# Performance work log

Hardware: AMD Instinct MI355X
Metric: run time of the kernel (lower is better)

Reference implementation:

```python
import jax, jax.numpy as jnp
import numpy as np

B, S, T = 512, 1024, 50


def setup_inputs() -> dict:
    key = jax.random.key(0)
    k1, k2, k3, k4, k5, k6, k7 = jax.random.split(key, 7)
    token_scores = jax.random.normal(k1, (B, S, T), dtype=jnp.float32)
    tags = jax.random.randint(k2, (B, S), 0, T, dtype=jnp.int64)
    # left-contiguous mask: each sequence has a random valid length >= 1
    lengths = jax.random.randint(k3, (B,), 1, S + 1)
    token_mask = (jnp.arange(S)[None, :] < lengths[:, None]).astype(jnp.int32)
    transitions = jax.random.normal(k4, (T, T), dtype=jnp.float32) * 0.1
    start_transitions = jax.random.normal(k5, (T,), dtype=jnp.float32) * 0.1
    end_transitions = jax.random.normal(k6, (T,), dtype=jnp.float32) * 0.1
    return {
        "token_scores": token_scores,
        "tags": tags,
        "token_mask": token_mask,
        "transitions": transitions,
        "start_transitions": start_transitions,
        "end_transitions": end_transitions,
    }


def _crf_log_likelihood(token_scores, tags, token_mask, transitions,
                        start_transitions, end_transitions):
    # token_scores: [B,S,T], tags: [B,S] int, token_mask: [B,S] {0,1}
    maskf = token_mask.astype(token_scores.dtype)
    maskb = token_mask.astype(bool)

    # ---- numerator: score of the gold tag path ----
    emit = jnp.take_along_axis(token_scores, tags[..., None], axis=2)[..., 0]  # [B,S]
    emit_sum = jnp.sum(emit * maskf, axis=1)
    trans_sum = jnp.sum(transitions[tags[:, :-1], tags[:, 1:]] * maskf[:, 1:], axis=1)
    start_score = start_transitions[tags[:, 0]]
    last_idx = jnp.sum(token_mask, axis=1).astype(jnp.int32) - 1          # [B]
    last_tags = jnp.take_along_axis(tags, last_idx[:, None], axis=1)[:, 0]
    end_score = end_transitions[last_tags]
    numerator = start_score + emit_sum + trans_sum + end_score            # [B]

    # ---- denominator: log partition via forward algorithm (scan over time) ----
    alpha0 = start_transitions[None, :] + token_scores[:, 0]              # [B,T]
    logits_rest = jnp.swapaxes(token_scores[:, 1:], 0, 1)                 # [S-1,B,T]
    mask_rest = jnp.swapaxes(maskb[:, 1:], 0, 1)                          # [S-1,B]

    def step(alpha, xs):
        logit_t, m_t = xs                                                 # [B,T], [B]
        # inner[b, i, j] = alpha[b,i] + transitions[i,j] + logit_t[b,j]
        inner = alpha[:, :, None] + transitions[None, :, :] + logit_t[:, None, :]
        new_alpha = jax.nn.logsumexp(inner, axis=1)                       # [B,T]
        alpha = jnp.where(m_t[:, None], new_alpha, alpha)
        return alpha, None

    alpha, _ = jax.lax.scan(step, alpha0, (logits_rest, mask_rest))
    denominator = jax.nn.logsumexp(alpha + end_transitions[None, :], axis=1)  # [B]

    return jnp.sum(numerator - denominator)  # scalar, summed over batch


def reference(token_scores, tags, token_mask, transitions,
              start_transitions, end_transitions):
    batch_size = token_scores.shape[0]
    ll = _crf_log_likelihood(token_scores, tags, token_mask, transitions,
                             start_transitions, end_transitions)
    return -ll / float(batch_size)
```

## Files before the change

kernel.cpp:

```cpp
#include <hip/hip_runtime.h>
#include <math.h>

#define CB 512
#define CS 1024
#define CT 50
#define PF 4

typedef float v2f __attribute__((ext_vector_type(2)));

#if __has_builtin(__builtin_amdgcn_permlane16_swap)
#define HAVE_PL16 1
#else
#define HAVE_PL16 0
#endif
#if __has_builtin(__builtin_amdgcn_permlane32_swap)
#define HAVE_PL32 1
#else
#define HAVE_PL32 0
#endif

__global__ void zero_out_kernel(float* out) { out[0] = 0.0f; }

__device__ __forceinline__ int lane0_bits(float v) {
    return __builtin_amdgcn_readlane(__float_as_int(v), 0);
}

template <int CTRL>
__device__ __forceinline__ float dppmov(float v) {
    return __int_as_float(__builtin_amdgcn_update_dpp(
        0, __float_as_int(v), CTRL, 0xf, 0xf, false));
}

__device__ __forceinline__ void expand32(float &a, float &b, int lane) {
#if HAVE_PL32
    (void)lane;
    auto r = __builtin_amdgcn_permlane32_swap(__float_as_uint(a), __float_as_uint(a),
                                              false, false);
    a = __uint_as_float(r[0]);
    b = __uint_as_float(r[1]);
#else
    b = __int_as_float(__builtin_amdgcn_ds_bpermute((lane ^ 32) << 2,
                                                    __float_as_int(a)));
#endif
}

__device__ __forceinline__ void expand16(float &a, float &b, int lane) {
    (void)lane;
#if HAVE_PL16
    auto r = __builtin_amdgcn_permlane16_swap(__float_as_uint(a), __float_as_uint(a),
                                              false, false);
    a = __uint_as_float(r[0]);
    b = __uint_as_float(r[1]);
#else
    b = __int_as_float(__builtin_amdgcn_ds_swizzle(__float_as_int(a), 0x401F));
#endif
}

__global__ __launch_bounds__(128, 1) void crf_scan_kernel(
    const float* __restrict__ scores,
    const int*   __restrict__ tags,
    const int*   __restrict__ mask,
    const float* __restrict__ trans,
    const float* __restrict__ start_tr,
    const float* __restrict__ end_tr,
    float* __restrict__ out)
{
    const int b    = blockIdx.x;
    const int tid  = threadIdx.x;
    const int w    = tid >> 6;
    const int lane = tid & 63;
    const int xl   = (lane < CT) ? lane : 0;
    const bool sel4 = (lane & 4) != 0;
    const bool sel8 = (lane & 8) != 0;

    __shared__ __attribute__((aligned(16))) float sTrans[CT * CT];
    __shared__ float sA[64];
    __shared__ float sB[64];
    __shared__ float sLZ[2], sN[2];

    for (int k = tid; k < CT * CT; k += 128) sTrans[k] = trans[k];
    __syncthreads();

    const int F16   = HAVE_PL16 ? (lane & 16) : 0;
    const int F32   = HAVE_PL32 ? (lane & 32) : 0;
    const int sbase = 16 * (lane >> 4) + (lane & 3);

    v2f EC0[16], EC1[16];
    #pragma unroll
    for (int k = 0; k < 16; ++k) {
        const int i = lane
            ^ ((k & 1) ? (32 ^ F32) : F32)
            ^ ((k & 2) ? (16 ^ F16) : F16)
            ^ ((k & 4) ? 1 : 0)
            ^ ((k & 8) ? 2 : 0);
        float e[4];
        #pragma unroll
        for (int u = 0; u < 4; ++u) {
            const int s = sbase + 4 * u;
            e[u] = (i < CT && s < CT)
                 ? __expf(w == 0 ? sTrans[i * CT + s] : sTrans[s * CT + i])
                 : 0.f;
        }
        EC0[k] = (v2f){e[0], e[1]};
        EC1[k] = (v2f){e[2], e[3]};
    }

    const int* mrow = mask + (size_t)b * CS;
    int len = 0;
    for (int t = lane; t < CS; t += 64) len += mrow[t];
    #pragma unroll
    for (int off = 32; off; off >>= 1) len += __shfl_xor(len, off);

    const float* srow = scores + (size_t)b * CS * CT;
    const float* sx   = srow + xl;

    const int tm    = (len - 1) >> 1;
    const int count = (w == 0) ? tm : ((len >= 2) ? (len - 2 - tm) : 0);
    const int base  = (w == 0) ? 1 : (len - 2);
    const int dir   = (w == 0) ? 1 : -1;

    float st;
    if (w == 0) {
        st = (lane < CT) ? __expf(start_tr[lane] + sx[0]) : 0.f;
    } else {
        st = (lane < CT)
            ? ((len >= 2) ? __expf(end_tr[lane] + sx[(size_t)(len - 1) * CT])
                          : __expf(end_tr[lane]))
            : 0.f;
    }
    int kexp = 0;

    #define MAC(k, gk, suf)                                                 \
    {                                                                       \
        const v2f t2 = {gk, gk};                                            \
        a0##suf = __builtin_elementwise_fma(t2, EC0[k], a0##suf);           \
        a1##suf = __builtin_elementwise_fma(t2, EC1[k], a1##suf);           \
    }

    #define STEP(EX)                                                        \
    {                                                                       \
        float g0 = st, g1, g2, g3;                                          \
        expand32(g0, g1, lane);                                             \
        expand16(g0, g2, lane);                                             \
        expand16(g1, g3, lane);                                             \
        const float g4  = dppmov<0xB1>(g0);                                 \
        const float g5  = dppmov<0xB1>(g1);                                 \
        const float g6  = dppmov<0xB1>(g2);                                 \
        const float g7  = dppmov<0xB1>(g3);                                 \
        const float g8  = dppmov<0x4E>(g0);                                 \
        const float g9  = dppmov<0x4E>(g1);                                 \
        const float g10 = dppmov<0x4E>(g2);                                 \
        const float g11 = dppmov<0x4E>(g3);                                 \
        const float g12 = dppmov<0x4E>(g4);                                 \
        const float g13 = dppmov<0x4E>(g5);                                 \
        const float g14 = dppmov<0x4E>(g6);                                 \
        const float g15 = dppmov<0x4E>(g7);                                 \
        v2f a0lo = {0.f, 0.f}, a1lo = {0.f, 0.f};                           \
        v2f a0hi = {0.f, 0.f}, a1hi = {0.f, 0.f};                           \
        MAC(0,  g0,  lo) MAC(1,  g1,  lo) MAC(2,  g2,  lo) MAC(3,  g3,  lo) \
        MAC(4,  g4,  lo) MAC(5,  g5,  lo) MAC(6,  g6,  lo) MAC(7,  g7,  lo) \
        MAC(8,  g8,  hi) MAC(9,  g9,  hi) MAC(10, g10, hi) MAC(11, g11, hi) \
        MAC(12, g12, hi) MAC(13, g13, hi) MAC(14, g14, hi) MAC(15, g15, hi) \
        v2f a0 = a0lo + a0hi;                                               \
        v2f a1 = a1lo + a1hi;                                               \
        a0.x += dppmov<0x124>(a0.x); a0.y += dppmov<0x124>(a0.y);           \
        a1.x += dppmov<0x124>(a1.x); a1.y += dppmov<0x124>(a1.y);           \
        a0.x += dppmov<0x128>(a0.x); a0.y += dppmov<0x128>(a0.y);           \
        a1.x += dppmov<0x128>(a1.x); a1.y += dppmov<0x128>(a1.y);           \
        const float o01 = sel4 ? a0.y : a0.x;                               \
        const float o23 = sel4 ? a1.y : a1.x;                               \
        st = (sel8 ? o23 : o01) * (EX);                                     \
    }

    #define RENORM()                                                        \
    {                                                                       \
        int sb = lane0_bits(st);                                            \
        int e  = (sb >> 23) & 0xff;                                         \
        kexp  += e - 127;                                                   \
        st    *= __int_as_float((254 - e) << 23);                           \
    }

    float xpf[PF];
    #pragma unroll
    for (int k = 0; k < PF; ++k) {
        int idx = base + dir * k;
        if (idx < 0) idx = 0;
        xpf[k] = sx[(size_t)idx * CT];
    }
    int k = 0;
    while (k + PF <= count) {
        float exk[PF];
        #pragma unroll
        for (int j = 0; j < PF; ++j) exk[j] = __expf(xpf[j]);
        #pragma unroll
        for (int j = 0; j < PF; ++j) {
            int idx = base + dir * (k + PF + j);
            if (idx < 0) idx = 0;
            xpf[j] = sx[(size_t)idx * CT];
        }
        RENORM();
        STEP(exk[0]); STEP(exk[1]); STEP(exk[2]); STEP(exk[3]);
        k += PF;
    }
    for (int r = 0; k < count; ++k, ++r) {
        float e = __expf(xpf[r]);
        RENORM();
        STEP(e);
    }
    if (w == 1 && len >= 2) { RENORM(); STEP(1.0f); }
    RENORM();
    #undef STEP
    #undef MAC
    #undef RENORM

    if (w == 0) sA[lane] = (lane < CT) ? st : 0.0f;
    else        sB[lane] = (lane < CT) ? st : 0.0f;
    if (lane == 0) sLZ[w] = (float)kexp * 0.6931471805599453f;
    __syncthreads();

    const int* trow = tags + (size_t)b * CS;
    float nsum = 0.0f;
    for (int t = tid; t < CS; t += 128) {
        if (t < len) {
            int tg = trow[t];
            nsum += srow[(size_t)t * CT + tg];
            if (t >= 1) nsum += sTrans[trow[t - 1] * CT + tg];
        }
    }
    #pragma unroll
    for (int off = 32; off; off >>= 1) nsum += __shfl_xor(nsum, off);
    if (lane == 0) sN[w] = nsum;

    float den = 0.0f;
    if (w == 0) {
        float vp = sA[lane] * sB[lane];
        #pragma unroll
        for (int off = 32; off; off >>= 1) vp += __shfl_xor(vp, off);
        den = sLZ[0] + sLZ[1] + __logf(vp);
    }
    __syncthreads();

    if (tid == 0) {
        float num = sN[0] + sN[1] + start_tr[trow[0]] + end_tr[trow[len - 1]];
        atomicAdd(out, (den - num) * (1.0f / CB));
    }
}

extern "C" void kernel_launch(void* const* d_in, const int* in_sizes, int n_in,
                              void* d_out, int out_size, void* d_ws, size_t ws_size,
                              hipStream_t stream) {
    const float* scores   = (const float*)d_in[0];
    const int*   tags     = (const int*)d_in[1];
    const int*   mask     = (const int*)d_in[2];
    const float* trans    = (const float*)d_in[3];
    const float* start_tr = (const float*)d_in[4];
    const float* end_tr   = (const float*)d_in[5];
    float* out = (float*)d_out;

    zero_out_kernel<<<1, 1, 0, stream>>>(out);
    crf_scan_kernel<<<CB, 128, 0, stream>>>(scores, tags, mask, trans,
                                            start_tr, end_tr, out);
}
```

Baseline: 305.8 us.

## Swap broadcast and reduction roles between DPP and permlane in CRF step

Restructures the per-step matrix-vector product so the 16-way broadcast of the state uses only DPP row shuffles (quad_perm and row_ror), while the cross-row reduction uses permlane32/16 swaps followed by adds. The exponentiated transition coefficients are re-laid out to match, with rotation offsets found at runtime by probing the DPP patterns. The aim is a shorter dependency chain per serial scan step, trading permlane expansions and row_ror reductions for a different mix. The risk is more permlane operations on the critical path (four values reduced twice each) and a dependence on the probed DPP rotation semantics being correct.

```diff
diff --git a/kernel.cpp b/kernel.cpp
--- a/kernel.cpp
+++ b/kernel.cpp
@@ -31,28 +31,28 @@
         0, __float_as_int(v), CTRL, 0xf, 0xf, false));
 }
 
-__device__ __forceinline__ void expand32(float &a, float &b, int lane) {
+__device__ __forceinline__ float pairsum32(float a, int lane) {
 #if HAVE_PL32
     (void)lane;
     auto r = __builtin_amdgcn_permlane32_swap(__float_as_uint(a), __float_as_uint(a),
                                               false, false);
-    a = __uint_as_float(r[0]);
-    b = __uint_as_float(r[1]);
-#else
-    b = __int_as_float(__builtin_amdgcn_ds_bpermute((lane ^ 32) << 2,
-                                                    __float_as_int(a)));
-#endif
-}
-
-__device__ __forceinline__ void expand16(float &a, float &b, int lane) {
+    return __uint_as_float(r[0]) + __uint_as_float(r[1]);
+#else
+    float b = __int_as_float(__builtin_amdgcn_ds_bpermute((lane ^ 32) << 2,
+                                                          __float_as_int(a)));
+    return a + b;
+#endif
+}
+
+__device__ __forceinline__ float pairsum16(float a, int lane) {
     (void)lane;
 #if HAVE_PL16
     auto r = __builtin_amdgcn_permlane16_swap(__float_as_uint(a), __float_as_uint(a),
                                               false, false);
-    a = __uint_as_float(r[0]);
-    b = __uint_as_float(r[1]);
-#else
-    b = __int_as_float(__builtin_amdgcn_ds_swizzle(__float_as_int(a), 0x401F));
+    return __uint_as_float(r[0]) + __uint_as_float(r[1]);
+#else
+    float b = __int_as_float(__builtin_amdgcn_ds_swizzle(__float_as_int(a), 0x401F));
+    return a + b;
 #endif
 }
 
@@ -70,8 +70,10 @@
     const int w    = tid >> 6;
     const int lane = tid & 63;
     const int xl   = (lane < CT) ? lane : 0;
-    const bool sel4 = (lane & 4) != 0;
-    const bool sel8 = (lane & 8) != 0;
+    const int j    = lane & 15;
+    const int rowb = lane & 48;
+    const bool sel16 = (lane & 16) != 0;
+    const bool sel32 = (lane & 32) != 0;
 
     __shared__ __attribute__((aligned(16))) float sTrans[CT * CT];
     __shared__ float sA[64];
@@ -81,28 +83,35 @@
     for (int k = tid; k < CT * CT; k += 128) sTrans[k] = trans[k];
     __syncthreads();
 
-    const int F16   = HAVE_PL16 ? (lane & 16) : 0;
-    const int F32   = HAVE_PL32 ? (lane & 32) : 0;
-    const int sbase = 16 * (lane >> 4) + (lane & 3);
-
-    v2f EC0[16], EC1[16];
-    #pragma unroll
-    for (int k = 0; k < 16; ++k) {
-        const int i = lane
-            ^ ((k & 1) ? (32 ^ F32) : F32)
-            ^ ((k & 2) ? (16 ^ F16) : F16)
-            ^ ((k & 4) ? 1 : 0)
-            ^ ((k & 8) ? 2 : 0);
-        float e[4];
-        #pragma unroll
-        for (int u = 0; u < 4; ++u) {
-            const int s = sbase + 4 * u;
-            e[u] = (i < CT && s < CT)
-                 ? __expf(w == 0 ? sTrans[i * CT + s] : sTrans[s * CT + i])
-                 : 0.f;
+    int d4, d8;
+    {
+        int p4 = __float_as_int(dppmov<0x124>(__int_as_float(lane)));
+        int p8 = __float_as_int(dppmov<0x128>(__int_as_float(lane)));
+        d4 = (p4 - lane) & 15;
+        d8 = (p8 - lane) & 15;
+    }
+
+    v2f EC01[16], EC23[16];
+    {
+        const int offs[4] = {0, d4, d8, (d4 + d8) & 15};
+        #pragma unroll
+        for (int a = 0; a < 4; ++a) {
+            #pragma unroll
+            for (int k = 0; k < 4; ++k) {
+                const int g = 4 * a + k;
+                const int i = rowb | (((j + offs[a]) & 15) ^ k);
+                float e[4];
+                #pragma unroll
+                for (int r = 0; r < 4; ++r) {
+                    const int s = 16 * r + j;
+                    e[r] = (i < CT && s < CT)
+                         ? __expf(w == 0 ? sTrans[i * CT + s] : sTrans[s * CT + i])
+                         : 0.f;
+                }
+                EC01[g] = (v2f){e[0], e[1]};
+                EC23[g] = (v2f){e[2], e[3]};
+            }
         }
-        EC0[k] = (v2f){e[0], e[1]};
-        EC1[k] = (v2f){e[2], e[3]};
     }
 
     const int* mrow = mask + (size_t)b * CS;
@@ -130,46 +139,48 @@
     }
     int kexp = 0;
 
-    #define MAC(k, gk, suf)                                                 \
-    {                                                                       \
-        const v2f t2 = {gk, gk};                                            \
-        a0##suf = __builtin_elementwise_fma(t2, EC0[k], a0##suf);           \
-        a1##suf = __builtin_elementwise_fma(t2, EC1[k], a1##suf);           \
-    }
-
     #define STEP(EX)                                                        \
     {                                                                       \
-        float g0 = st, g1, g2, g3;                                          \
-        expand32(g0, g1, lane);                                             \
-        expand16(g0, g2, lane);                                             \
-        expand16(g1, g3, lane);                                             \
-        const float g4  = dppmov<0xB1>(g0);                                 \
-        const float g5  = dppmov<0xB1>(g1);                                 \
-        const float g6  = dppmov<0xB1>(g2);                                 \
-        const float g7  = dppmov<0xB1>(g3);                                 \
-        const float g8  = dppmov<0x4E>(g0);                                 \
-        const float g9  = dppmov<0x4E>(g1);                                 \
-        const float g10 = dppmov<0x4E>(g2);                                 \
-        const float g11 = dppmov<0x4E>(g3);                                 \
-        const float g12 = dppmov<0x4E>(g4);                                 \
-        const float g13 = dppmov<0x4E>(g5);                                 \
-        const float g14 = dppmov<0x4E>(g6);                                 \
-        const float g15 = dppmov<0x4E>(g7);                                 \
-        v2f a0lo = {0.f, 0.f}, a1lo = {0.f, 0.f};                           \
-        v2f a0hi = {0.f, 0.f}, a1hi = {0.f, 0.f};                           \
-        MAC(0,  g0,  lo) MAC(1,  g1,  lo) MAC(2,  g2,  lo) MAC(3,  g3,  lo) \
-        MAC(4,  g4,  lo) MAC(5,  g5,  lo) MAC(6,  g6,  lo) MAC(7,  g7,  lo) \
-        MAC(8,  g8,  hi) MAC(9,  g9,  hi) MAC(10, g10, hi) MAC(11, g11, hi) \
-        MAC(12, g12, hi) MAC(13, g13, hi) MAC(14, g14, hi) MAC(15, g15, hi) \
-        v2f a0 = a0lo + a0hi;                                               \
-        v2f a1 = a1lo + a1hi;                                               \
-        a0.x += dppmov<0x124>(a0.x); a0.y += dppmov<0x124>(a0.y);           \
-        a1.x += dppmov<0x124>(a1.x); a1.y += dppmov<0x124>(a1.y);           \
-        a0.x += dppmov<0x128>(a0.x); a0.y += dppmov<0x128>(a0.y);           \
-        a1.x += dppmov<0x128>(a1.x); a1.y += dppmov<0x128>(a1.y);           \
-        const float o01 = sel4 ? a0.y : a0.x;                               \
-        const float o23 = sel4 ? a1.y : a1.x;                               \
-        st = (sel8 ? o23 : o01) * (EX);                                     \
+        float G[16];                                                        \
+        G[0]  = st;                                                         \
+        G[1]  = dppmov<0xB1>(st);                                           \
+        G[2]  = dppmov<0x4E>(st);                                           \
+        G[3]  = dppmov<0x4E>(G[1]);                                         \
+        G[4]  = dppmov<0x124>(G[0]);                                        \
+        G[5]  = dppmov<0x124>(G[1]);                                        \
+        G[6]  = dppmov<0x124>(G[2]);                                        \
+        G[7]  = dppmov<0x124>(G[3]);                                        \
+        G[8]  = dppmov<0x128>(G[0]);                                        \
+        G[9]  = dppmov<0x128>(G[1]);                                        \
+        G[10] = dppmov<0x128>(G[2]);                                        \
+        G[11] = dppmov<0x128>(G[3]);                                        \
+        G[12] = dppmov<0x128>(G[4]);                                        \
+        G[13] = dppmov<0x128>(G[5]);                                        \
+        G[14] = dppmov<0x128>(G[6]);                                        \
+        G[15] = dppmov<0x128>(G[7]);                                        \
+        v2f q01a = {0.f,0.f}, q01b = {0.f,0.f};                             \
+        v2f q23a = {0.f,0.f}, q23b = {0.f,0.f};                             \
+        _Pragma("unroll")                                                   \
+        for (int g = 0; g < 8; ++g) {                                       \
+            const v2f t2 = {G[g], G[g]};                                    \
+            q01a = __builtin_elementwise_fma(t2, EC01[g], q01a);            \
+            q23a = __builtin_elementwise_fma(t2, EC23[g], q23a);            \
+        }                                                                   \
+        _Pragma("unroll")                                                   \
+        for (int g = 8; g < 16; ++g) {                                      \
+            const v2f t2 = {G[g], G[g]};                                    \
+            q01b = __builtin_elementwise_fma(t2, EC01[g], q01b);            \
+            q23b = __builtin_elementwise_fma(t2, EC23[g], q23b);            \
+        }                                                                   \
+        const v2f Q01 = q01a + q01b;                                        \
+        const v2f Q23 = q23a + q23b;                                        \
+        const float Y0 = pairsum16(pairsum32(Q01.x, lane), lane);           \
+        const float Y1 = pairsum16(pairsum32(Q01.y, lane), lane);           \
+        const float Y2 = pairsum16(pairsum32(Q23.x, lane), lane);           \
+        const float Y3 = pairsum16(pairsum32(Q23.y, lane), lane);           \
+        const float u0 = sel16 ? Y1 : Y0;                                   \
+        const float u1 = sel16 ? Y3 : Y2;                                   \
+        st = (sel32 ? u1 : u0) * (EX);                                      \
     }
 
     #define RENORM()                                                        \
@@ -191,12 +202,12 @@
     while (k + PF <= count) {
         float exk[PF];
         #pragma unroll
-        for (int j = 0; j < PF; ++j) exk[j] = __expf(xpf[j]);
-        #pragma unroll
-        for (int j = 0; j < PF; ++j) {
-            int idx = base + dir * (k + PF + j);
+        for (int jj = 0; jj < PF; ++jj) exk[jj] = __expf(xpf[jj]);
+        #pragma unroll
+        for (int jj = 0; jj < PF; ++jj) {
+            int idx = base + dir * (k + PF + jj);
             if (idx < 0) idx = 0;
-            xpf[j] = sx[(size_t)idx * CT];
+            xpf[jj] = sx[(size_t)idx * CT];
         }
         RENORM();
         STEP(exk[0]); STEP(exk[1]); STEP(exk[2]); STEP(exk[3]);
@@ -210,7 +221,6 @@
     if (w == 1 && len >= 2) { RENORM(); STEP(1.0f); }
     RENORM();
     #undef STEP
-    #undef MAC
     #undef RENORM
 
     if (w == 0) sA[lane] = (lane < CT) ? st : 0.0f;
```

After: 343.4 us. +12.3%, slower.
